# Performance work log

Measured on AMD Instinct MI355X. Metric: run time of the kernel, lower is better.

## Reference

```python
import jax, jax.numpy as jnp
import numpy as np

N_NODES = 8192
K = 32

def setup_inputs() -> dict:
    key = jax.random.key(0)
    kA, kI = jax.random.split(key)
    A = jax.random.normal(kA, (N_NODES, N_NODES), dtype=jnp.float32)
    idx = jnp.arange(N_NODES, dtype=jnp.int64)  # unused by forward, kept for signature fidelity
    return {"A": A, "idx": idx}

def reference(A, idx):
    # adj = relu(A)
    adj = jax.nn.relu(A)
    # row-wise top-k indices, scatter 1.0 into a zero mask, multiply
    _, indices = jax.lax.top_k(adj, K)            # [N, K]
    rows = jnp.arange(adj.shape[0])[:, None]      # [N, 1]
    mask = jnp.zeros_like(adj).at[rows, indices].set(1.0)
    return adj * mask
```

## Files before the change

kernel.cpp:

```cpp
#include <hip/hip_runtime.h>


constexpr int N     = 8192;
constexpr int K     = 32;
constexpr int NBINS = 2048;
constexpr int SPEC_BASE = 1024;
constexpr int CAP   = 512;
constexpr int SLOTS = CAP / 64;
constexpr int BB    = 128;
constexpr int BLOCK = 256;
constexpr float TSPEC = 2.0f;

typedef float f4 __attribute__((ext_vector_type(4)));

template<int PER>
__device__ __forceinline__ bool find_cutoff(const unsigned* hist, int lane,
                                            int base, int& B, int& G) {
    unsigned s = 0;
    #pragma unroll
    for (int i = 0; i < PER; ++i)
        s += hist[base + lane * PER + ((i + lane) & (PER - 1))];
    unsigned acc = s;
    #pragma unroll
    for (int off = 1; off < 64; off <<= 1) {
        unsigned t = __shfl_down(acc, off, 64);
        if (lane + off < 64) acc += t;
    }
    unsigned long long m = __ballot(acc >= (unsigned)K);
    if (m == 0ull) return false;
    int g = 63 - __clzll((long long)m);
    unsigned above = (g < 63) ? (unsigned)__shfl((int)acc, g + 1, 64) : 0u;
    unsigned h  = (lane < PER) ? hist[base + g * PER + lane] : 0u;
    unsigned a2 = h;
    #pragma unroll
    for (int off = 1; off < 64; off <<= 1) {
        unsigned t = __shfl_down(a2, off, 64);
        if (lane + off < 64) a2 += t;
    }
    unsigned long long m2 = __ballot(above + a2 >= (unsigned)K);
    int bl = 63 - __clzll((long long)m2);
    B = base + g * PER + bl;
    G = (int)(above + (unsigned)__shfl((int)a2, bl, 64)
                    - (unsigned)__shfl((int)h,  bl, 64));
    return true;
}

__global__ __launch_bounds__(BLOCK)
void topk_relu_kernel(const float* __restrict__ A, float* __restrict__ Out) {
    const int row  = blockIdx.x;
    const int tid  = threadIdx.x;
    const int lane = tid & 63;

    __shared__ unsigned hist[NBINS];
    __shared__ float    cv[CAP];
    __shared__ int      cc[CAP];
    __shared__ float    bbv[BB];
    __shared__ int      bbc[BB];
    __shared__ unsigned ccnt;

    #pragma unroll
    for (int i = 0; i < (NBINS - SPEC_BASE) / BLOCK; ++i)
        hist[SPEC_BASE + tid + i * BLOCK] = 0u;
    if (tid == 0) ccnt = 0u;
    __syncthreads();

    const f4* __restrict__ Arow = reinterpret_cast<const f4*>(A + (size_t)row * N);
    #pragma unroll
    for (int i = 0; i < 8; ++i) {
        f4 v = Arow[i * BLOCK + tid];
        #pragma unroll
        for (int c = 0; c < 4; ++c) {
            float f = v[c];
            if (f > TSPEC) {
                atomicAdd(&hist[__float_as_uint(f) >> 20], 1u);
                unsigned ix = atomicAdd(&ccnt, 1u);
                if (ix < CAP) { cv[ix] = f; cc[ix] = (i * BLOCK + tid) * 4 + c; }
            }
        }
    }
    __syncthreads();

    int B, G;
    bool ok = find_cutoff<16>(hist, lane, SPEC_BASE, B, G);
    unsigned Call = ccnt;
    if (!ok || Call > (unsigned)CAP) {
        __syncthreads();
        #pragma unroll
        for (int i = 0; i < NBINS / BLOCK; ++i) hist[tid + i * BLOCK] = 0u;
        if (tid == 0) ccnt = 0u;
        __syncthreads();
        #pragma unroll
        for (int i = 0; i < 8; ++i) {
            f4 v = Arow[i * BLOCK + tid];
            #pragma unroll
            for (int c = 0; c < 4; ++c) {
                float f = v[c];
                if (f > 0.0f) atomicAdd(&hist[__float_as_uint(f) >> 20], 1u);
            }
        }
        __syncthreads();
        if (!find_cutoff<32>(hist, lane, 0, B, G)) { B = -1; G = 0; }
        if (B >= 0) {
            #pragma unroll
            for (int i = 0; i < 8; ++i) {
                f4 v = Arow[i * BLOCK + tid];
                #pragma unroll
                for (int c = 0; c < 4; ++c) {
                    float f = v[c];
                    if (f > 0.0f && (int)(__float_as_uint(f) >> 20) == B) {
                        unsigned ix = atomicAdd(&ccnt, 1u);
                        if (ix < CAP) { cv[ix] = f; cc[ix] = (i * BLOCK + tid) * 4 + c; }
                    }
                }
            }
        }
        __syncthreads();
        Call = ccnt;
    }
    const int R = K - G;

    float vR = 0.0f;
    int   cR = -1;
    if (B >= 0) {
        const int C = (int)min(Call, (unsigned)CAP);
        int total = 0;
        #pragma unroll
        for (int s = 0; s < SLOTS; ++s) {
            const int j = lane + s * 64;
            bool flag = false; float fv = 0.0f; int fc = 0;
            if (j < C) {
                fv = cv[j];
                if ((int)(__float_as_uint(fv) >> 20) == B) { flag = true; fc = cc[j]; }
            }
            unsigned long long m = __ballot(flag);
            if (flag) {
                int pos = total + __popcll(m & ((1ull << lane) - 1ull));
                if (pos < BB) { bbv[pos] = fv; bbc[pos] = fc; }
            }
            total += (int)__popcll(m);
        }
        const int T = min(total, BB);
        float mv0 = -1.0f, mv1 = -1.0f; int mc0 = 0x7fffffff, mc1 = 0x7fffffff;
        if (lane      < T) { mv0 = bbv[lane];      mc0 = bbc[lane]; }
        if (lane + 64 < T) { mv1 = bbv[lane + 64]; mc1 = bbc[lane + 64]; }
        int r0 = 0, r1 = 0;
        for (int j = 0; j < T; ++j) {
            const float vj = bbv[j];
            const int   cj = bbc[j];
            if (vj > mv0 || (vj == mv0 && cj < mc0)) r0++;
            if (vj > mv1 || (vj == mv1 && cj < mc1)) r1++;
        }
        float bv = 0.0f; int bc = -1; bool found = false;
        if (lane      < T && r0 == R - 1) { bv = mv0; bc = mc0; found = true; }
        if (lane + 64 < T && r1 == R - 1) { bv = mv1; bc = mc1; found = true; }
        vR = __int_as_float(0x7f800000);
        unsigned long long bm = __ballot(found);
        if (bm != 0ull) {
            int src = (int)__ffsll((long long)bm) - 1;
            vR = __shfl(bv, src, 64);
            cR = __shfl(bc, src, 64);
        }
    }

    float* __restrict__ Orow = Out + (size_t)row * N;
    #pragma unroll
    for (int i = 0; i < 8; ++i) {
        f4 v = Arow[i * BLOCK + tid];
        f4 w;
        #pragma unroll
        for (int c = 0; c < 4; ++c) {
            float f   = v[c];
            int   col = (i * BLOCK + tid) * 4 + c;
            w[c] = ((f > vR) || (f == vR && col <= cR)) ? f : 0.0f;
        }
        __builtin_nontemporal_store(w, reinterpret_cast<f4*>(Orow) + i * BLOCK + tid);
    }
}

extern "C" void kernel_launch(void* const* d_in, const int* in_sizes, int n_in,
                              void* d_out, int out_size, void* d_ws, size_t ws_size,
                              hipStream_t stream) {
    const float* A   = (const float*)d_in[0];
    float*       Out = (float*)d_out;
    (void)in_sizes; (void)n_in; (void)d_ws; (void)ws_size; (void)out_size;
    topk_relu_kernel<<<dim3(N), dim3(BLOCK), 0, stream>>>(A, Out);
}
```

Before: 108.6 us.

## Write zeros then scatter selected candidates instead of re-reading the row

In the common speculative path, each block now streams zeros to its output row and then has one wave scatter the surviving top-k values from the shared candidate list. This avoids a second pass over the input row for the final masked write. The rare fallback path is reorganised to rank all bucket candidates directly, with a per-lane register array. The approach depends on the zero stores and the later scattered stores to the same addresses being ordered across threads by the barrier, which is a correctness risk.

```diff
diff --git a/kernel.cpp b/kernel.cpp
--- a/kernel.cpp
+++ b/kernel.cpp
@@ -50,6 +50,7 @@
     const int row  = blockIdx.x;
     const int tid  = threadIdx.x;
     const int lane = tid & 63;
+    const int wave = tid >> 6;
 
     __shared__ unsigned hist[NBINS];
     __shared__ float    cv[CAP];
@@ -82,47 +83,17 @@
 
     int B, G;
     bool ok = find_cutoff<16>(hist, lane, SPEC_BASE, B, G);
-    unsigned Call = ccnt;
-    if (!ok || Call > (unsigned)CAP) {
-        __syncthreads();
-        #pragma unroll
-        for (int i = 0; i < NBINS / BLOCK; ++i) hist[tid + i * BLOCK] = 0u;
-        if (tid == 0) ccnt = 0u;
-        __syncthreads();
-        #pragma unroll
-        for (int i = 0; i < 8; ++i) {
-            f4 v = Arow[i * BLOCK + tid];
-            #pragma unroll
-            for (int c = 0; c < 4; ++c) {
-                float f = v[c];
-                if (f > 0.0f) atomicAdd(&hist[__float_as_uint(f) >> 20], 1u);
-            }
-        }
-        __syncthreads();
-        if (!find_cutoff<32>(hist, lane, 0, B, G)) { B = -1; G = 0; }
-        if (B >= 0) {
-            #pragma unroll
-            for (int i = 0; i < 8; ++i) {
-                f4 v = Arow[i * BLOCK + tid];
-                #pragma unroll
-                for (int c = 0; c < 4; ++c) {
-                    float f = v[c];
-                    if (f > 0.0f && (int)(__float_as_uint(f) >> 20) == B) {
-                        unsigned ix = atomicAdd(&ccnt, 1u);
-                        if (ix < CAP) { cv[ix] = f; cc[ix] = (i * BLOCK + tid) * 4 + c; }
-                    }
-                }
-            }
-        }
-        __syncthreads();
-        Call = ccnt;
-    }
-    const int R = K - G;
-
-    float vR = 0.0f;
-    int   cR = -1;
-    if (B >= 0) {
-        const int C = (int)min(Call, (unsigned)CAP);
+    const unsigned Call = ccnt;
+    f4* __restrict__ Orow4 = reinterpret_cast<f4*>(Out + (size_t)row * N);
+
+    if (ok && Call <= (unsigned)CAP) {
+        const f4 z = {0.0f, 0.0f, 0.0f, 0.0f};
+        #pragma unroll
+        for (int i = 0; i < 8; ++i)
+            __builtin_nontemporal_store(z, Orow4 + i * BLOCK + tid);
+
+        const int R = K - G;
+        const int C = (int)Call;
         int total = 0;
         #pragma unroll
         for (int s = 0; s < SLOTS; ++s) {
@@ -153,6 +124,87 @@
         float bv = 0.0f; int bc = -1; bool found = false;
         if (lane      < T && r0 == R - 1) { bv = mv0; bc = mc0; found = true; }
         if (lane + 64 < T && r1 == R - 1) { bv = mv1; bc = mc1; found = true; }
+        float vR = __int_as_float(0x7f800000);
+        int   cR = -1;
+        unsigned long long bm = __ballot(found);
+        if (bm != 0ull) {
+            int src = (int)__ffsll((long long)bm) - 1;
+            vR = __shfl(bv, src, 64);
+            cR = __shfl(bc, src, 64);
+        }
+
+        __syncthreads();
+
+        if (wave == 0) {
+            float* __restrict__ Orow = Out + (size_t)row * N;
+            #pragma unroll
+            for (int s = 0; s < SLOTS; ++s) {
+                const int j = lane + s * 64;
+                if (j < C) {
+                    float f = cv[j]; int c = cc[j];
+                    if (f > vR || (f == vR && c <= cR)) Orow[c] = f;
+                }
+            }
+        }
+        return;
+    }
+
+    __syncthreads();
+    #pragma unroll
+    for (int i = 0; i < NBINS / BLOCK; ++i) hist[tid + i * BLOCK] = 0u;
+    if (tid == 0) ccnt = 0u;
+    __syncthreads();
+    #pragma unroll
+    for (int i = 0; i < 8; ++i) {
+        f4 v = Arow[i * BLOCK + tid];
+        #pragma unroll
+        for (int c = 0; c < 4; ++c) {
+            float f = v[c];
+            if (f > 0.0f) atomicAdd(&hist[__float_as_uint(f) >> 20], 1u);
+        }
+    }
+    __syncthreads();
+    if (!find_cutoff<32>(hist, lane, 0, B, G)) { B = -1; G = 0; }
+    if (B >= 0) {
+        #pragma unroll
+        for (int i = 0; i < 8; ++i) {
+            f4 v = Arow[i * BLOCK + tid];
+            #pragma unroll
+            for (int c = 0; c < 4; ++c) {
+                float f = v[c];
+                if (f > 0.0f && (int)(__float_as_uint(f) >> 20) == B) {
+                    unsigned ix = atomicAdd(&ccnt, 1u);
+                    if (ix < CAP) { cv[ix] = f; cc[ix] = (i * BLOCK + tid) * 4 + c; }
+                }
+            }
+        }
+    }
+    __syncthreads();
+
+    float vR = 0.0f;
+    int   cR = -1;
+    if (B >= 0) {
+        const int R = K - G;
+        const int C = (int)min(ccnt, (unsigned)CAP);
+        float mv[SLOTS]; int mc[SLOTS]; int rk[SLOTS];
+        #pragma unroll
+        for (int s = 0; s < SLOTS; ++s) {
+            const int j = lane + s * 64;
+            if (j < C) { mv[s] = cv[j]; mc[s] = cc[j]; }
+            else       { mv[s] = -1.0f; mc[s] = 0x7fffffff; }
+            rk[s] = 0;
+        }
+        for (int j = 0; j < C; ++j) {
+            const float vj = cv[j];
+            const int   cj = cc[j];
+            #pragma unroll
+            for (int s = 0; s < SLOTS; ++s)
+                if (vj > mv[s] || (vj == mv[s] && cj < mc[s])) rk[s]++;
+        }
+        float bv = 0.0f; int bc = -1; bool found = false;
+        #pragma unroll
+        for (int s = 0; s < SLOTS; ++s)
+            if (lane + s * 64 < C && rk[s] == R - 1) { bv = mv[s]; bc = mc[s]; found = true; }
         vR = __int_as_float(0x7f800000);
         unsigned long long bm = __ballot(found);
         if (bm != 0ull) {
@@ -162,7 +214,6 @@
         }
     }
 
-    float* __restrict__ Orow = Out + (size_t)row * N;
     #pragma unroll
     for (int i = 0; i < 8; ++i) {
         f4 v = Arow[i * BLOCK + tid];
@@ -173,7 +224,7 @@
             int   col = (i * BLOCK + tid) * 4 + c;
             w[c] = ((f > vR) || (f == vR && col <= cR)) ? f : 0.0f;
         }
-        __builtin_nontemporal_store(w, reinterpret_cast<f4*>(Orow) + i * BLOCK + tid);
+        __builtin_nontemporal_store(w, Orow4 + i * BLOCK + tid);
     }
 }
 
```

Result: faster. 104.7 us (-3.6%).
